# Kernel optimization log

Hardware: AMD Instinct MI355X
Metric: run time of the kernel (lower is better)

## Reference

```python
import jax, jax.numpy as jnp
import numpy as np

N_NODES = 100000
N_EDGES = 1600000
D_FEAT = 50
ALPHA = 0.1


def setup_inputs() -> dict:
    key = jax.random.key(0)
    k1, k2, k3, k4, k5 = jax.random.split(key, 5)
    x = jax.random.normal(k1, (N_NODES, D_FEAT), dtype=jnp.float32)
    h = jax.random.normal(k2, (N_NODES, D_FEAT), dtype=jnp.float32)
    adj_vals = jax.random.uniform(k3, (N_EDGES,), dtype=jnp.float32)
    adj_rows = jax.random.randint(k4, (N_EDGES,), 0, N_NODES, dtype=jnp.int32)
    adj_cols = jax.random.randint(k5, (N_EDGES,), 0, N_NODES, dtype=jnp.int32)
    return {"x": x, "h": h, "adj_vals": adj_vals,
            "adj_rows": adj_rows, "adj_cols": adj_cols}


def reference(x, h, adj_vals, adj_rows, adj_cols):
    # SpMM: out[r] += vals[e] * x[cols[e]] for edges e with rows[e] == r.
    # Equivalent to the original per-column torch.sparse.mm loop, fused.
    msgs = adj_vals[:, None] * x[adj_cols]          # [E, d] gather + scale
    ax = jax.ops.segment_sum(msgs, adj_rows, num_segments=N_NODES)  # [N, d]
    return (1.0 - ALPHA) * ax + ALPHA * h
```

## Files before the change

kernel.cpp:

```cpp
#include <hip/hip_runtime.h>
#include <hip/hip_bf16.h>

#define N_NODES 100000
#define N_EDGES 1600000
#define D_FEAT 50
#define ALPHA 0.1f

#define BINSHIFT 6
#define BINROWS 64
#define NBINS ((N_NODES + BINROWS - 1) / BINROWS)
#define CAP 1280
#define SCK 2560
#define NSCB ((N_EDGES + SCK - 1) / SCK)
#define XB_STRIDE 64
#define SCAN_ITEMS ((NBINS + 63) / 64)

__global__ void init_out_kernel(const float* __restrict__ h,
                                float* __restrict__ out, int n) {
    int idx = blockIdx.x * blockDim.x + threadIdx.x;
    if (idx < n) out[idx] = ALPHA * h[idx];
}

__global__ void scatter_atomic_kernel(const float* __restrict__ x,
                                      const float* __restrict__ vals,
                                      const int* __restrict__ rows,
                                      const int* __restrict__ cols,
                                      float* __restrict__ out) {
    long long idx = (long long)blockIdx.x * blockDim.x + threadIdx.x;
    long long total = (long long)N_EDGES * D_FEAT;
    if (idx >= total) return;
    int e = (int)(idx / D_FEAT);
    int d = (int)(idx % D_FEAT);
    float contrib = (1.0f - ALPHA) * vals[e] * x[(long long)cols[e] * D_FEAT + d];
    atomicAdd(&out[(long long)rows[e] * D_FEAT + d], contrib);
}


__global__ __launch_bounds__(256) void cvt_init_kernel(const float* __restrict__ x,
                                                       ushort* __restrict__ xb,
                                                       int* __restrict__ bin_cursor) {
    int i = blockIdx.x * 256 + threadIdx.x;
    if (i < NBINS) bin_cursor[i] = i * CAP;
    if (i >= N_NODES * XB_STRIDE) return;
    int r = i >> 6, d = i & (XB_STRIDE - 1);
    float v = (d < D_FEAT) ? x[r * D_FEAT + d] : 0.0f;
    unsigned u = __float_as_uint(v);
    unsigned rnd = (u + 0x7FFFu + ((u >> 16) & 1u)) >> 16;
    xb[i] = (ushort)rnd;
}

__global__ __launch_bounds__(512) void bin_scatter_kernel(
        const float* __restrict__ vals,
        const int* __restrict__ rows,
        const int* __restrict__ cols,
        int* __restrict__ bin_cursor,
        float2* __restrict__ packed) {
    __shared__ float2 sbuf[SCK];
    __shared__ ushort sbin[SCK];
    __shared__ int lh[NBINS];
    __shared__ int lws[NBINS];
    __shared__ int gbase[NBINS];
    int t = threadIdx.x;
    int cs = blockIdx.x * SCK;
    int ce = cs + SCK;
    if (ce > N_EDGES) ce = N_EDGES;
    int cn = ce - cs;
    for (int i = t; i < NBINS; i += 512) lh[i] = 0;
    __syncthreads();
    for (int e = cs + t; e < ce; e += 512)
        atomicAdd(&lh[rows[e] >> BINSHIFT], 1);
    __syncthreads();
    if (t < 64) {
        int base = t * SCAN_ITEMS;
        int loc[SCAN_ITEMS];
        int s2 = 0;
        #pragma unroll
        for (int i = 0; i < SCAN_ITEMS; ++i) {
            int idx = base + i;
            int c = (idx < NBINS) ? lh[idx] : 0;
            loc[i] = s2; s2 += c;
        }
        int incl = s2;
        #pragma unroll
        for (int off = 1; off < 64; off <<= 1) {
            int u = __shfl_up(incl, off);
            if (t >= off) incl += u;
        }
        int excl = incl - s2;
        #pragma unroll
        for (int i = 0; i < SCAN_ITEMS; ++i) {
            int idx = base + i;
            if (idx < NBINS) lws[idx] = excl + loc[i];
        }
    }
    __syncthreads();
    for (int i = t; i < NBINS; i += 512) {
        int c = lh[i];
        gbase[i] = c ? atomicAdd(&bin_cursor[i], c) : 0;
        lh[i] = lws[i];
    }
    __syncthreads();
    for (int e = cs + t; e < ce; e += 512) {
        int r = rows[e];
        int b = r >> BINSHIFT;
        int pos = atomicAdd(&lh[b], 1);
        float2 p;
        p.x = __int_as_float(((r & (BINROWS - 1)) << 17) | cols[e]);
        p.y = vals[e] * (1.0f - ALPHA);
        sbuf[pos] = p;
        sbin[pos] = (ushort)b;
    }
    __syncthreads();
    for (int j = t; j < cn; j += 512) {
        int b = sbin[j];
        packed[gbase[b] + (j - lws[b])] = sbuf[j];
    }
}

__global__ __launch_bounds__(512) void spmm_fused_kernel(
        const ushort* __restrict__ xb,
        const float* __restrict__ h,
        const int* __restrict__ bin_cursor,
        const float2* __restrict__ packed,
        float* __restrict__ out) {
    __shared__ float2 ebuf[CAP];
    __shared__ float2 srt[CAP];
    __shared__ int rstart[BINROWS];
    __shared__ int cur[BINROWS];
    __shared__ int cnt[BINROWS];
    int bin = blockIdx.x;
    int t = threadIdx.x;
    int gb = bin * CAP;
    int n = bin_cursor[bin] - gb;
    if (n > CAP) n = CAP;
    if (n < 0) n = 0;
    if (t < BINROWS) cnt[t] = 0;
    __syncthreads();
    for (int i = t; i < n; i += 512) {
        float2 p = packed[gb + i];
        ebuf[i] = p;
        atomicAdd(&cnt[__float_as_int(p.x) >> 17], 1);
    }
    __syncthreads();
    if (t < 64) {
        int c = cnt[t];
        int incl = c;
        #pragma unroll
        for (int off = 1; off < 64; off <<= 1) {
            int u = __shfl_up(incl, off);
            if (t >= off) incl += u;
        }
        rstart[t] = incl - c;
        cur[t] = incl - c;
    }
    __syncthreads();
    for (int i = t; i < n; i += 512) {
        float2 p = ebuf[i];
        int pk = __float_as_int(p.x);
        int pos = atomicAdd(&cur[pk >> 17], 1);
        float2 q;
        q.x = __int_as_float(pk & 0x1FFFF);
        q.y = p.y;
        srt[pos] = q;
    }
    __syncthreads();
    int lane = t & 63;
    int wv = t >> 6;
    int half = lane >> 5;
    int fl = lane & 31;
    int r0 = bin << BINSHIFT;
    for (int r = wv; r < BINROWS; r += 8) {
        int gr = r0 + r;
        if (gr >= N_NODES) break;
        int es = rstart[r];
        int ee = es + cnt[r];
        float a0 = 0.0f, a1 = 0.0f, b0 = 0.0f, b1 = 0.0f;
        int ei = es;
        for (; ei + 4 <= ee; ei += 4) {
            float2 p = srt[ei + half];
            float2 q = srt[ei + 2 + half];
            int cp = __float_as_int(p.x);
            int cq = __float_as_int(q.x);
            unsigned wp = *(const unsigned*)(xb + (cp << 6) + 2 * fl);
            unsigned wq = *(const unsigned*)(xb + (cq << 6) + 2 * fl);
            a0 += p.y * __uint_as_float(wp << 16);
            a1 += p.y * __uint_as_float(wp & 0xFFFF0000u);
            b0 += q.y * __uint_as_float(wq << 16);
            b1 += q.y * __uint_as_float(wq & 0xFFFF0000u);
        }
        for (; ei < ee; ei += 2) {
            int idx = ei + half;
            bool valid = idx < ee;
            float2 p = srt[valid ? idx : es];
            float v = valid ? p.y : 0.0f;
            int cp = __float_as_int(p.x);
            unsigned wp = *(const unsigned*)(xb + (cp << 6) + 2 * fl);
            a0 += v * __uint_as_float(wp << 16);
            a1 += v * __uint_as_float(wp & 0xFFFF0000u);
        }
        a0 += b0;
        a1 += b1;
        a0 += __shfl_xor(a0, 32);
        a1 += __shfl_xor(a1, 32);
        if (lane < D_FEAT / 2) {
            int o = gr * D_FEAT + 2 * fl;
            float2 hv = *(const float2*)(h + o);
            float2 rr;
            rr.x = a0 + ALPHA * hv.x;
            rr.y = a1 + ALPHA * hv.y;
            *(float2*)(out + o) = rr;
        }
    }
}

extern "C" void kernel_launch(void* const* d_in, const int* in_sizes, int n_in,
                              void* d_out, int out_size, void* d_ws, size_t ws_size,
                              hipStream_t stream) {
    const float* x        = (const float*)d_in[0];
    const float* h        = (const float*)d_in[1];
    const float* adj_vals = (const float*)d_in[2];
    const int*   adj_rows = (const int*)d_in[3];
    const int*   adj_cols = (const int*)d_in[4];
    float* out = (float*)d_out;

    size_t n_ints = (size_t)NBINS;
    n_ints = (n_ints + 1) & ~(size_t)1;
    size_t needed = n_ints * 4 + (size_t)NBINS * CAP * 8
                  + (size_t)N_NODES * XB_STRIDE * 2;

    if (ws_size < needed) {
        int n_out = N_NODES * D_FEAT;
        init_out_kernel<<<(n_out + 255) / 256, 256, 0, stream>>>(h, out, n_out);
        long long total = (long long)N_EDGES * D_FEAT;
        scatter_atomic_kernel<<<(int)((total + 255) / 256), 256, 0, stream>>>(
            x, adj_vals, adj_rows, adj_cols, out);
        return;
    }

    int* bin_cursor = (int*)d_ws;
    float2* packed  = (float2*)((int*)d_ws + n_ints);
    ushort* xb      = (ushort*)(packed + (size_t)NBINS * CAP);

    cvt_init_kernel<<<(N_NODES * XB_STRIDE + 255) / 256, 256, 0, stream>>>(
        x, xb, bin_cursor);
    bin_scatter_kernel<<<NSCB, 512, 0, stream>>>(
        adj_vals, adj_rows, adj_cols, bin_cursor, packed);
    spmm_fused_kernel<<<NBINS, 512, 0, stream>>>(
        xb, h, bin_cursor, packed, out);
}
```

Baseline: 200.8 us.

## Enlarge scatter chunks, shrink SpMM blocks, drop LDS staging, unroll gather by 8

The bin scatter kernel now uses 1024-thread blocks over 5120-edge chunks, which halves the block count and the number of global cursor atomics. The SpMM kernel drops from 512 to 256 threads and removes the ebuf shared staging buffer. It re-reads packed edges from global memory in the second pass instead, cutting LDS use so more blocks can fit per CU. The row gather loop gains an 8-way unrolled path to put more independent loads in flight. Risks: larger scatter chunks need more LDS and lower scatter occupancy, and the packed data is now read twice from global memory.

```diff
diff --git a/kernel.cpp b/kernel.cpp
--- a/kernel.cpp
+++ b/kernel.cpp
@@ -10,7 +10,7 @@
 #define BINROWS 64
 #define NBINS ((N_NODES + BINROWS - 1) / BINROWS)
 #define CAP 1280
-#define SCK 2560
+#define SCK 5120
 #define NSCB ((N_EDGES + SCK - 1) / SCK)
 #define XB_STRIDE 64
 #define SCAN_ITEMS ((NBINS + 63) / 64)
@@ -49,7 +49,7 @@
     xb[i] = (ushort)rnd;
 }
 
-__global__ __launch_bounds__(512) void bin_scatter_kernel(
+__global__ __launch_bounds__(1024) void bin_scatter_kernel(
         const float* __restrict__ vals,
         const int* __restrict__ rows,
         const int* __restrict__ cols,
@@ -65,9 +65,9 @@
     int ce = cs + SCK;
     if (ce > N_EDGES) ce = N_EDGES;
     int cn = ce - cs;
-    for (int i = t; i < NBINS; i += 512) lh[i] = 0;
-    __syncthreads();
-    for (int e = cs + t; e < ce; e += 512)
+    for (int i = t; i < NBINS; i += 1024) lh[i] = 0;
+    __syncthreads();
+    for (int e = cs + t; e < ce; e += 1024)
         atomicAdd(&lh[rows[e] >> BINSHIFT], 1);
     __syncthreads();
     if (t < 64) {
@@ -94,13 +94,13 @@
         }
     }
     __syncthreads();
-    for (int i = t; i < NBINS; i += 512) {
+    for (int i = t; i < NBINS; i += 1024) {
         int c = lh[i];
         gbase[i] = c ? atomicAdd(&bin_cursor[i], c) : 0;
         lh[i] = lws[i];
     }
     __syncthreads();
-    for (int e = cs + t; e < ce; e += 512) {
+    for (int e = cs + t; e < ce; e += 1024) {
         int r = rows[e];
         int b = r >> BINSHIFT;
         int pos = atomicAdd(&lh[b], 1);
@@ -111,19 +111,18 @@
         sbin[pos] = (ushort)b;
     }
     __syncthreads();
-    for (int j = t; j < cn; j += 512) {
+    for (int j = t; j < cn; j += 1024) {
         int b = sbin[j];
         packed[gbase[b] + (j - lws[b])] = sbuf[j];
     }
 }
 
-__global__ __launch_bounds__(512) void spmm_fused_kernel(
+__global__ __launch_bounds__(256) void spmm_fused_kernel(
         const ushort* __restrict__ xb,
         const float* __restrict__ h,
         const int* __restrict__ bin_cursor,
         const float2* __restrict__ packed,
         float* __restrict__ out) {
-    __shared__ float2 ebuf[CAP];
     __shared__ float2 srt[CAP];
     __shared__ int rstart[BINROWS];
     __shared__ int cur[BINROWS];
@@ -136,11 +135,8 @@
     if (n < 0) n = 0;
     if (t < BINROWS) cnt[t] = 0;
     __syncthreads();
-    for (int i = t; i < n; i += 512) {
-        float2 p = packed[gb + i];
-        ebuf[i] = p;
-        atomicAdd(&cnt[__float_as_int(p.x) >> 17], 1);
-    }
+    for (int i = t; i < n; i += 256)
+        atomicAdd(&cnt[__float_as_int(packed[gb + i].x) >> 17], 1);
     __syncthreads();
     if (t < 64) {
         int c = cnt[t];
@@ -154,8 +150,8 @@
         cur[t] = incl - c;
     }
     __syncthreads();
-    for (int i = t; i < n; i += 512) {
-        float2 p = ebuf[i];
+    for (int i = t; i < n; i += 256) {
+        float2 p = packed[gb + i];
         int pk = __float_as_int(p.x);
         int pos = atomicAdd(&cur[pk >> 17], 1);
         float2 q;
@@ -169,20 +165,36 @@
     int half = lane >> 5;
     int fl = lane & 31;
     int r0 = bin << BINSHIFT;
-    for (int r = wv; r < BINROWS; r += 8) {
+    for (int r = wv; r < BINROWS; r += 4) {
         int gr = r0 + r;
         if (gr >= N_NODES) break;
         int es = rstart[r];
         int ee = es + cnt[r];
         float a0 = 0.0f, a1 = 0.0f, b0 = 0.0f, b1 = 0.0f;
         int ei = es;
+        for (; ei + 8 <= ee; ei += 8) {
+            float2 p = srt[ei + half];
+            float2 q = srt[ei + 2 + half];
+            float2 r2 = srt[ei + 4 + half];
+            float2 s2 = srt[ei + 6 + half];
+            unsigned wp = *(const unsigned*)(xb + ((__float_as_int(p.x)) << 6) + 2 * fl);
+            unsigned wq = *(const unsigned*)(xb + ((__float_as_int(q.x)) << 6) + 2 * fl);
+            unsigned wr = *(const unsigned*)(xb + ((__float_as_int(r2.x)) << 6) + 2 * fl);
+            unsigned ws = *(const unsigned*)(xb + ((__float_as_int(s2.x)) << 6) + 2 * fl);
+            a0 += p.y * __uint_as_float(wp << 16);
+            a1 += p.y * __uint_as_float(wp & 0xFFFF0000u);
+            b0 += q.y * __uint_as_float(wq << 16);
+            b1 += q.y * __uint_as_float(wq & 0xFFFF0000u);
+            a0 += r2.y * __uint_as_float(wr << 16);
+            a1 += r2.y * __uint_as_float(wr & 0xFFFF0000u);
+            b0 += s2.y * __uint_as_float(ws << 16);
+            b1 += s2.y * __uint_as_float(ws & 0xFFFF0000u);
+        }
         for (; ei + 4 <= ee; ei += 4) {
             float2 p = srt[ei + half];
             float2 q = srt[ei + 2 + half];
-            int cp = __float_as_int(p.x);
-            int cq = __float_as_int(q.x);
-            unsigned wp = *(const unsigned*)(xb + (cp << 6) + 2 * fl);
-            unsigned wq = *(const unsigned*)(xb + (cq << 6) + 2 * fl);
+            unsigned wp = *(const unsigned*)(xb + ((__float_as_int(p.x)) << 6) + 2 * fl);
+            unsigned wq = *(const unsigned*)(xb + ((__float_as_int(q.x)) << 6) + 2 * fl);
             a0 += p.y * __uint_as_float(wp << 16);
             a1 += p.y * __uint_as_float(wp & 0xFFFF0000u);
             b0 += q.y * __uint_as_float(wq << 16);
@@ -193,8 +205,7 @@
             bool valid = idx < ee;
             float2 p = srt[valid ? idx : es];
             float v = valid ? p.y : 0.0f;
-            int cp = __float_as_int(p.x);
-            unsigned wp = *(const unsigned*)(xb + (cp << 6) + 2 * fl);
+            unsigned wp = *(const unsigned*)(xb + ((__float_as_int(p.x)) << 6) + 2 * fl);
             a0 += v * __uint_as_float(wp << 16);
             a1 += v * __uint_as_float(wp & 0xFFFF0000u);
         }
@@ -243,8 +254,8 @@
 
     cvt_init_kernel<<<(N_NODES * XB_STRIDE + 255) / 256, 256, 0, stream>>>(
         x, xb, bin_cursor);
-    bin_scatter_kernel<<<NSCB, 512, 0, stream>>>(
+    bin_scatter_kernel<<<NSCB, 1024, 0, stream>>>(
         adj_vals, adj_rows, adj_cols, bin_cursor, packed);
-    spmm_fused_kernel<<<NBINS, 512, 0, stream>>>(
+    spmm_fused_kernel<<<NBINS, 256, 0, stream>>>(
         xb, h, bin_cursor, packed, out);
 }
```

Result: faster. 185.2 us (-7.8%).
